# Kernel tuning notes

Measured on AMD Instinct MI355X. Metric: run time of the kernel, lower is better.

The kernel has to match this reference:

```python
import jax, jax.numpy as jnp
import numpy as np

D_MODEL = 1024
NUM_HEADS = 16
HEAD_DIM = D_MODEL // NUM_HEADS  # 64
D_FF = 4096
EPS = 1e-5


def layer_norm(x, gamma, beta):
    mu = jnp.mean(x, axis=-1, keepdims=True)
    var = jnp.mean((x - mu) ** 2, axis=-1, keepdims=True)
    return (x - mu) * jax.lax.rsqrt(var + EPS) * gamma + beta


def apply_rope(t):
    # t: [B, H, S, head_dim]; interleaved-pair rotation as in RoPE.apply_rope
    S, d = t.shape[-2], t.shape[-1]
    inv_freq = 1.0 / (10000.0 ** (jnp.arange(0, d, 2, dtype=jnp.float32) / d))  # [d/2]
    angles = jnp.arange(S, dtype=jnp.float32)[:, None] * inv_freq[None, :]      # [S, d/2]
    sin, cos = jnp.sin(angles), jnp.cos(angles)
    tp = t.reshape(*t.shape[:-1], d // 2, 2)  # pairs of adjacent elements
    t0, t1 = tp[..., 0], tp[..., 1]
    rot = jnp.stack([t0 * cos - t1 * sin, t0 * sin + t1 * cos], axis=-1)
    return rot.reshape(t.shape)


def setup_inputs() -> dict:
    key = jax.random.key(0)
    ks = jax.random.split(key, 18)
    s = 0.02
    d, f = D_MODEL, D_FF
    return {
        "x": jax.random.normal(ks[0], (2, 2048, d), dtype=jnp.float32),
        "Wq": jax.random.normal(ks[1], (d, d), dtype=jnp.float32) * s,
        "bq": jnp.zeros((d,), jnp.float32),
        "Wk": jax.random.normal(ks[2], (d, d), dtype=jnp.float32) * s,
        "bk": jnp.zeros((d,), jnp.float32),
        "Wv": jax.random.normal(ks[3], (d, d), dtype=jnp.float32) * s,
        "bv": jnp.zeros((d,), jnp.float32),
        "Wo": jax.random.normal(ks[4], (d, d), dtype=jnp.float32) * s,
        "bo": jnp.zeros((d,), jnp.float32),
        "W1": jax.random.normal(ks[5], (d, f), dtype=jnp.float32) * s,
        "b1": jnp.zeros((f,), jnp.float32),
        "W2": jax.random.normal(ks[6], (f, d), dtype=jnp.float32) * s,
        "b2": jnp.zeros((d,), jnp.float32),
        "g1": jnp.ones((d,), jnp.float32),
        "beta1": jnp.zeros((d,), jnp.float32),
        "g2": jnp.ones((d,), jnp.float32),
        "beta2": jnp.zeros((d,), jnp.float32),
    }


def reference(x, Wq, bq, Wk, bk, Wv, bv, Wo, bo, W1, b1, W2, b2, g1, beta1, g2, beta2):
    B, S, d = x.shape
    H, hd = NUM_HEADS, HEAD_DIM
    x_norm = layer_norm(x, g1, beta1)
    q = (x_norm @ Wq + bq).reshape(B, S, H, hd).transpose(0, 2, 1, 3)  # [B,H,S,hd]
    k = (x_norm @ Wk + bk).reshape(B, S, H, hd).transpose(0, 2, 1, 3)
    v = (x_norm @ Wv + bv).reshape(B, S, H, hd).transpose(0, 2, 1, 3)
    q = apply_rope(q)
    k = apply_rope(k)
    q = q * (1.0 / jnp.sqrt(jnp.float32(hd)))
    scores = jnp.einsum("bhqd,bhkd->bhqk", q, k)  # [B,H,S,S]
    attn = jax.nn.softmax(scores, axis=-1)
    out = jnp.einsum("bhqk,bhkd->bhqd", attn, v)
    out = out.transpose(0, 2, 1, 3).reshape(B, S, d)
    attn_out = out @ Wo + bo
    x = x + attn_out  # dropout p=0 (eval)
    x_norm2 = layer_norm(x, g2, beta2)
    ffn = jax.nn.relu(x_norm2 @ W1 + b1) @ W2 + b2
    return x + ffn
```

## Files before the change

kernel.cpp:

```cpp
#include <hip/hip_runtime.h>

typedef unsigned short bf16_t;
typedef short short8 __attribute__((ext_vector_type(8)));
typedef float f32x4 __attribute__((ext_vector_type(4)));
typedef float f32x16 __attribute__((ext_vector_type(16)));
typedef unsigned int u32x4 __attribute__((ext_vector_type(4)));

static __device__ __forceinline__ unsigned short f2bf(float f) {
  unsigned int u = __float_as_uint(f);
  unsigned int r = (u + 0x7FFFu + ((u >> 16) & 1u)) >> 16;
  return (unsigned short)r;
}
static __device__ __forceinline__ float bf2f(unsigned short u) {
  return __uint_as_float((unsigned int)u << 16);
}
static __device__ __forceinline__ unsigned int cvt_pk_bf16(float lo, float hi) {
  unsigned int r;
  asm("v_cvt_pk_bf16_f32 %0, %1, %2" : "=v"(r) : "v"(lo), "v"(hi));
  return r;
}
static __device__ __forceinline__ void pl32swap(unsigned int& a, unsigned int& b) {
  asm("v_permlane32_swap_b32 %0, %1" : "+v"(a), "+v"(b));
}

__device__ __forceinline__ void gload_lds16(const void* g, void* l) {
  __builtin_amdgcn_global_load_lds((const __attribute__((address_space(1))) void*)g,
                                   (__attribute__((address_space(3))) void*)l,
                                   16, 0, 0);
}

__global__ __launch_bounds__(256) void prep_kernel(
    const float* __restrict__ Wq, const float* __restrict__ Wk,
    const float* __restrict__ Wv, const float* __restrict__ Wo,
    const float* __restrict__ W1, const float* __restrict__ W2,
    const float* __restrict__ x, const float* __restrict__ g1,
    const float* __restrict__ be1,
    bf16_t* __restrict__ WqkvT, bf16_t* __restrict__ W1T,
    bf16_t* __restrict__ W2T, bf16_t* __restrict__ xnb) {
  __shared__ float tile[32][33];
  const int bid = blockIdx.x;
  if (bid < 12288) {
    const float* src;
    bf16_t* dst;
    int rows, cols, bx, by;
    if (bid < 4096) {
      const int z = bid >> 10, r = bid & 1023;
      src = (z == 0) ? Wq : (z == 1) ? Wk : (z == 2) ? Wv : Wo;
      dst = WqkvT + (size_t)z * 1048576;
      rows = 1024; cols = 1024;
      bx = (r & 31) * 32; by = (r >> 5) * 32;
    } else if (bid < 8192) {
      const int r = bid - 4096;
      src = W1; dst = W1T; rows = 1024; cols = 4096;
      bx = (r & 127) * 32; by = (r >> 7) * 32;
    } else {
      const int r = bid - 8192;
      src = W2; dst = W2T; rows = 4096; cols = 1024;
      bx = (r & 31) * 32; by = (r >> 5) * 32;
    }
    const int tx = threadIdx.x & 31, ty = threadIdx.x >> 5;
#pragma unroll
    for (int i = 0; i < 32; i += 8)
      tile[ty + i][tx] = src[(size_t)(by + ty + i) * cols + (bx + tx)];
    __syncthreads();
#pragma unroll
    for (int i = 0; i < 32; i += 8)
      dst[(size_t)(bx + ty + i) * rows + (by + tx)] = f2bf(tile[tx][ty + i]);
  } else {
    const int row = bid - 12288;
    const int tid = threadIdx.x;
    const float4 v = reinterpret_cast<const float4*>(x + (size_t)row * 1024)[tid];
    float s = v.x + v.y + v.z + v.w;
    float ss = v.x * v.x + v.y * v.y + v.z * v.z + v.w * v.w;
#pragma unroll
    for (int off = 32; off; off >>= 1) {
      s += __shfl_xor(s, off, 64);
      ss += __shfl_xor(ss, off, 64);
    }
    float* red = &tile[0][0];
    const int wave = tid >> 6, lane = tid & 63;
    if (lane == 0) { red[wave] = s; red[4 + wave] = ss; }
    __syncthreads();
    const float mu = (red[0] + red[1] + red[2] + red[3]) * (1.f / 1024.f);
    const float ms = (red[4] + red[5] + red[6] + red[7]) * (1.f / 1024.f);
    const float rstd = rsqrtf(ms - mu * mu + 1e-5f);
    const float4 gg = reinterpret_cast<const float4*>(g1)[tid];
    const float4 bb = reinterpret_cast<const float4*>(be1)[tid];
    bf16_t* o = xnb + (size_t)row * 1024 + tid * 4;
    o[0] = f2bf((v.x - mu) * rstd * gg.x + bb.x);
    o[1] = f2bf((v.y - mu) * rstd * gg.y + bb.y);
    o[2] = f2bf((v.z - mu) * rstd * gg.z + bb.z);
    o[3] = f2bf((v.w - mu) * rstd * gg.w + bb.w);
  }
}

__global__ __launch_bounds__(256) void ln2_combine(const bf16_t* __restrict__ p,
                                                   const float* __restrict__ x,
                                                   const float* __restrict__ bo,
                                                   const float* __restrict__ g,
                                                   const float* __restrict__ be,
                                                   float* __restrict__ x2,
                                                   bf16_t* __restrict__ xn) {
  const int row = blockIdx.x;
  const int tid = threadIdx.x;
  const float4 xv = reinterpret_cast<const float4*>(x + (size_t)row * 1024)[tid];
  const float4 bb = reinterpret_cast<const float4*>(bo)[tid];
  float4 v = {bb.x + xv.x, bb.y + xv.y, bb.z + xv.z, bb.w + xv.w};
#pragma unroll
  for (int z = 0; z < 4; ++z) {
    const ushort4 a = reinterpret_cast<const ushort4*>(p + (size_t)z * 4194304 + (size_t)row * 1024)[tid];
    v.x += bf2f(a.x); v.y += bf2f(a.y); v.z += bf2f(a.z); v.w += bf2f(a.w);
  }
  reinterpret_cast<float4*>(x2 + (size_t)row * 1024)[tid] = v;
  float s = v.x + v.y + v.z + v.w;
  float ss = v.x * v.x + v.y * v.y + v.z * v.z + v.w * v.w;
#pragma unroll
  for (int off = 32; off; off >>= 1) {
    s += __shfl_xor(s, off, 64);
    ss += __shfl_xor(ss, off, 64);
  }
  __shared__ float red[8];
  const int wave = tid >> 6, lane = tid & 63;
  if (lane == 0) { red[wave] = s; red[4 + wave] = ss; }
  __syncthreads();
  const float mu = (red[0] + red[1] + red[2] + red[3]) * (1.f / 1024.f);
  const float ms = (red[4] + red[5] + red[6] + red[7]) * (1.f / 1024.f);
  const float rstd = rsqrtf(ms - mu * mu + 1e-5f);
  const float4 gg = reinterpret_cast<const float4*>(g)[tid];
  const float4 eb = reinterpret_cast<const float4*>(be)[tid];
  bf16_t* o = xn + (size_t)row * 1024 + tid * 4;
  o[0] = f2bf((v.x - mu) * rstd * gg.x + eb.x);
  o[1] = f2bf((v.y - mu) * rstd * gg.y + eb.y);
  o[2] = f2bf((v.z - mu) * rstd * gg.z + eb.z);
  o[3] = f2bf((v.w - mu) * rstd * gg.w + eb.w);
}

__global__ __launch_bounds__(256) void ffn_combine(const bf16_t* __restrict__ p0,
                                                   const bf16_t* __restrict__ p2,
                                                   const float* __restrict__ x2,
                                                   const float* __restrict__ b2,
                                                   float* __restrict__ out) {
  const int row = blockIdx.x;
  const int tid = threadIdx.x;
  const ushort4 a0 = reinterpret_cast<const ushort4*>(p0 + (size_t)row * 1024)[tid];
  const ushort4 a1 = reinterpret_cast<const ushort4*>(p0 + 4194304 + (size_t)row * 1024)[tid];
  const ushort4 a2 = reinterpret_cast<const ushort4*>(p2 + (size_t)row * 1024)[tid];
  const float4 xv = reinterpret_cast<const float4*>(x2 + (size_t)row * 1024)[tid];
  const float4 bb = reinterpret_cast<const float4*>(b2)[tid];
  float4 v;
  v.x = bf2f(a0.x) + bf2f(a1.x) + bf2f(a2.x) + bb.x + xv.x;
  v.y = bf2f(a0.y) + bf2f(a1.y) + bf2f(a2.y) + bb.y + xv.y;
  v.z = bf2f(a0.z) + bf2f(a1.z) + bf2f(a2.z) + bb.z + xv.z;
  v.w = bf2f(a0.w) + bf2f(a1.w) + bf2f(a2.w) + bb.w + xv.w;
  reinterpret_cast<float4*>(out + (size_t)row * 1024)[tid] = v;
}

__global__ __launch_bounds__(256) void rope_bf16(bf16_t* __restrict__ q,
                                                 bf16_t* __restrict__ k) {
  const int id = blockIdx.x * 256 + threadIdx.x;
  const int i = id & 31;
  const int s = (id >> 5) & 2047;
  const int bh = id >> 16;
  const float inv = exp2f((float)i * -0.41524101186f);
  float sn, cs;
  sincosf((float)s * inv, &sn, &cs);
  const size_t base = ((size_t)bh * 2048 + s) * 64 + 2 * i;
  unsigned int qp = *(unsigned int*)&q[base];
  unsigned int kp = *(unsigned int*)&k[base];
  const float q0 = bf2f(qp & 0xffff), q1 = bf2f(qp >> 16);
  const float k0 = bf2f(kp & 0xffff), k1 = bf2f(kp >> 16);
  const float qs = 0.18033688f;
  const unsigned int qo =
      (unsigned int)f2bf((q0 * cs - q1 * sn) * qs) |
      ((unsigned int)f2bf((q0 * sn + q1 * cs) * qs) << 16);
  const unsigned int ko =
      (unsigned int)f2bf(k0 * cs - k1 * sn) |
      ((unsigned int)f2bf(k0 * sn + k1 * cs) << 16);
  *(unsigned int*)&q[base] = qo;
  *(unsigned int*)&k[base] = ko;
}

__global__ __launch_bounds__(256) void vtrans(const bf16_t* __restrict__ v,
                                              bf16_t* __restrict__ vt) {
  __shared__ bf16_t tile[32][33];
  const int bh = blockIdx.x;
  const int s0 = blockIdx.y * 32;
  const int d0 = blockIdx.z * 32;
  const int tx = threadIdx.x & 31, ty = threadIdx.x >> 5;
  const size_t base = (size_t)bh * (2048 * 64);
#pragma unroll
  for (int i = 0; i < 32; i += 8)
    tile[ty + i][tx] = v[base + (size_t)(s0 + ty + i) * 64 + d0 + tx];
  __syncthreads();
#pragma unroll
  for (int i = 0; i < 32; i += 8)
    vt[base + (size_t)(d0 + ty + i) * 2048 + s0 + tx] = tile[tx][ty + i];
}

__global__ __launch_bounds__(256) void attn4(const bf16_t* __restrict__ qb,
                                             const bf16_t* __restrict__ kb,
                                             const bf16_t* __restrict__ vt,
                                             bf16_t* __restrict__ out) {
  const int bh = blockIdx.x;
  const int tid = threadIdx.x, wave = tid >> 6, lane = tid & 63;
  const int l31 = lane & 31, hi = lane >> 5;
  const int q0 = blockIdx.y * 128 + wave * 32;
  const size_t kvb = (size_t)bh * (2048 * 64);

  __shared__ __align__(16) bf16_t Ks[2][4096];
  __shared__ __align__(16) bf16_t Vs[2][4096];
  __shared__ float lred[4][32];

  short8 qf[4];
#pragma unroll
  for (int st = 0; st < 4; ++st)
    qf[st] = *(const short8*)&qb[kvb + (size_t)(q0 + l31) * 64 + st * 16 + hi * 8];

  f32x16 acc0, acc1;
#pragma unroll
  for (int r = 0; r < 16; ++r) { acc0[r] = 0.f; acc1[r] = 0.f; }
  float ls0 = 0.f, ls1 = 0.f, ls2 = 0.f, ls3 = 0.f;

#pragma unroll
  for (int j = 0; j < 2; ++j) {
    const int s = wave * 128 + j * 64 + lane;
    const int r = s >> 3;
    const int c = (s & 7) ^ (r & 7);
    gload_lds16(kb + kvb + (size_t)r * 64 + c * 8, &Ks[0][(size_t)s * 8]);
    gload_lds16(vt + kvb + (size_t)r * 2048 + c * 8, &Vs[0][(size_t)s * 8]);
  }
  __syncthreads();

  for (int t = 0; t < 2048; t += 64) {
    const int cur = (t >> 6) & 1;
    if (t + 64 < 2048) {
#pragma unroll
      for (int j = 0; j < 2; ++j) {
        const int s = wave * 128 + j * 64 + lane;
        const int r = s >> 3;
        const int c = (s & 7) ^ (r & 7);
        gload_lds16(kb + kvb + (size_t)(t + 64 + r) * 64 + c * 8, &Ks[cur ^ 1][(size_t)s * 8]);
        gload_lds16(vt + kvb + (size_t)r * 2048 + (t + 64) + c * 8, &Vs[cur ^ 1][(size_t)s * 8]);
      }
    }
    f32x16 p0, p1;
#pragma unroll
    for (int r = 0; r < 16; ++r) { p0[r] = 0.f; p1[r] = 0.f; }
#pragma unroll
    for (int st = 0; st < 4; ++st) {
      const int R0 = l31, R1 = 32 + l31;
      const short8 kf0 = *(const short8*)&Ks[cur][(size_t)(R0 * 8 + (((st << 1) | hi) ^ (R0 & 7))) * 8];
      const short8 kf1 = *(const short8*)&Ks[cur][(size_t)(R1 * 8 + (((st << 1) | hi) ^ (R1 & 7))) * 8];
      p0 = __builtin_amdgcn_mfma_f32_32x32x16_bf16(kf0, qf[st], p0, 0, 0, 0);
      p1 = __builtin_amdgcn_mfma_f32_32x32x16_bf16(kf1, qf[st], p1, 0, 0, 0);
    }
#pragma unroll
    for (int f = 0; f < 2; ++f) {
      f32x16& p = f ? p1 : p0;
      float e[16];
#pragma unroll
      for (int r = 0; r < 16; ++r) e[r] = exp2f(p[r]);
      ls0 += e[0] + e[1] + e[2] + e[3];
      ls1 += e[4] + e[5] + e[6] + e[7];
      ls2 += e[8] + e[9] + e[10] + e[11];
      ls3 += e[12] + e[13] + e[14] + e[15];
      unsigned int a0 = cvt_pk_bf16(e[0], e[1]), b0 = cvt_pk_bf16(e[4], e[5]);
      unsigned int a1 = cvt_pk_bf16(e[2], e[3]), b1 = cvt_pk_bf16(e[6], e[7]);
      unsigned int a2 = cvt_pk_bf16(e[8], e[9]), b2 = cvt_pk_bf16(e[12], e[13]);
      unsigned int a3 = cvt_pk_bf16(e[10], e[11]), b3 = cvt_pk_bf16(e[14], e[15]);
      pl32swap(a0, b0);
      pl32swap(a1, b1);
      pl32swap(a2, b2);
      pl32swap(a3, b3);
      const u32x4 w0 = {a0, a1, b0, b1};
      const u32x4 w1 = {a2, a3, b2, b3};
      const short8 pf0 = __builtin_bit_cast(short8, w0);
      const short8 pf1 = __builtin_bit_cast(short8, w1);
#pragma unroll
      for (int ks = 0; ks < 2; ++ks) {
        const short8 pf = ks ? pf1 : pf0;
        {
          const int R = l31;
          const int C = (((f << 2) | (ks << 1) | hi) ^ (R & 7));
          const short8 vf = *(const short8*)&Vs[cur][(size_t)(R * 8 + C) * 8];
          acc0 = __builtin_amdgcn_mfma_f32_32x32x16_bf16(pf, vf, acc0, 0, 0, 0);
        }
        {
          const int R = 32 + l31;
          const int C = (((f << 2) | (ks << 1) | hi) ^ (R & 7));
          const short8 vf = *(const short8*)&Vs[cur][(size_t)(R * 8 + C) * 8];
          acc1 = __builtin_amdgcn_mfma_f32_32x32x16_bf16(pf, vf, acc1, 0, 0, 0);
        }
      }
    }
    __syncthreads();
  }

  float lsum = (ls0 + ls1) + (ls2 + ls3);
  lsum += __shfl_xor(lsum, 32, 64);
  if (lane < 32) lred[wave][l31] = lsum;
  __syncthreads();

  const int b = bh >> 4, h = bh & 15;
#pragma unroll
  for (int r = 0; r < 16; ++r) {
    const int qrow = (r & 3) + 8 * (r >> 2) + 4 * hi;
    const float rl = 1.f / lred[wave][qrow];
    const size_t ro = (size_t)(b * 2048 + q0 + qrow) * 1024 + h * 64;
    out[ro + l31] = f2bf(acc0[r] * rl);
    out[ro + 32 + l31] = f2bf(acc1[r] * rl);
  }
}

enum { MODE_QKV = 0, MODE_FF1 = 1, MODE_PART = 2 };

template <int MODE>
__global__ __launch_bounds__(256) void gemm_bt(
    const bf16_t* __restrict__ A, const bf16_t* __restrict__ BT,
    int M, int N, int K, int kspan,
    const float* __restrict__ bias0, const float* __restrict__ bias1,
    const float* __restrict__ bias2,
    bf16_t* __restrict__ ob0, bf16_t* __restrict__ ob1, bf16_t* __restrict__ ob2) {
  __shared__ __align__(16) char smem[34816];
  bf16_t* As = (bf16_t*)smem;
  bf16_t* Bs = (bf16_t*)(smem + 16384);
  const int tid = threadIdx.x;
  const int wave = tid >> 6, lane = tid & 63;
  const int row16 = lane & 15, quad = lane >> 4;
  const int m0 = blockIdx.x * 128, n0 = blockIdx.y * 128;
  const int wm = (wave & 1) << 6, wn = (wave >> 1) << 6;

  f32x4 acc[4][4];
#pragma unroll
  for (int i = 0; i < 4; ++i)
#pragma unroll
    for (int j = 0; j < 4; ++j) acc[i][j] = (f32x4){0.f, 0.f, 0.f, 0.f};

  const int kb = blockIdx.z * kspan;
  const int kend = (kb + kspan < K) ? kb + kspan : K;

  for (int k0 = kb; k0 < kend; k0 += 64) {
#pragma unroll
    for (int j = 0; j < 4; ++j) {
      const int s = j * 256 + tid;
      const int r = s >> 3;
      const int cg = ((s & 7) ^ (r & 7)) << 3;
      gload_lds16(A + (size_t)(m0 + r) * K + k0 + cg, As + (size_t)s * 8);
      gload_lds16(BT + (size_t)(n0 + r) * K + k0 + cg, Bs + (size_t)s * 8);
    }
    __syncthreads();
    const int sw = row16 & 7;
#pragma unroll
    for (int kk = 0; kk < 2; ++kk) {
      short8 af[4], bfr[4];
#pragma unroll
      for (int mi = 0; mi < 4; ++mi)
        af[mi] = *(const short8*)&As[(size_t)(wm + mi * 16 + row16) * 64 + (((kk << 2) | quad) ^ sw) * 8];
#pragma unroll
      for (int ni = 0; ni < 4; ++ni)
        bfr[ni] = *(const short8*)&Bs[(size_t)(wn + ni * 16 + row16) * 64 + (((kk << 2) | quad) ^ sw) * 8];
#pragma unroll
      for (int mi = 0; mi < 4; ++mi)
#pragma unroll
        for (int ni = 0; ni < 4; ++ni)
          acc[mi][ni] =
              __builtin_amdgcn_mfma_f32_16x16x32_bf16(af[mi], bfr[ni], acc[mi][ni], 0, 0, 0);
    }
    __syncthreads();
  }

  bf16_t* ct = (bf16_t*)smem;
#pragma unroll
  for (int mi = 0; mi < 4; ++mi)
#pragma unroll
    for (int ni = 0; ni < 4; ++ni) {
      const int gn = n0 + wn + ni * 16 + row16;
      float bsv = 0.f;
      if (MODE == MODE_QKV)
        bsv = (gn < 1024) ? bias0[gn] : (gn < 2048) ? bias1[gn - 1024] : bias2[gn - 2048];
      else if (MODE == MODE_FF1)
        bsv = bias0[gn];
#pragma unroll
      for (int r = 0; r < 4; ++r) {
        float c = acc[mi][ni][r] + bsv;
        if (MODE == MODE_FF1) c = fmaxf(c, 0.f);
        ct[(size_t)(wm + mi * 16 + quad * 4 + r) * 136 + wn + ni * 16 + row16] = f2bf(c);
      }
    }
  __syncthreads();
  const int lr0 = tid >> 4, lc = tid & 15;
#pragma unroll
  for (int i = 0; i < 8; ++i) {
    const int lr = i * 16 + lr0;
    const uint4 v = *(const uint4*)&ct[(size_t)lr * 136 + lc * 8];
    const int gm = m0 + lr;
    if (MODE == MODE_QKV) {
      const int nn = (n0 & 1023) + lc * 8;
      const int h = nn >> 6, d = nn & 63;
      const int b = gm >> 11, s = gm & 2047;
      bf16_t* dst = (n0 < 1024) ? ob0 : (n0 < 2048) ? ob1 : ob2;
      *(uint4*)&dst[(((size_t)b * 16 + h) * 2048 + s) * 64 + d] = v;
    } else if (MODE == MODE_FF1) {
      *(uint4*)&ob0[(size_t)gm * N + n0 + lc * 8] = v;
    } else {
      bf16_t* dst = (blockIdx.z == 2) ? ob1 : ob0 + (size_t)blockIdx.z * 4194304;
      *(uint4*)&dst[(size_t)gm * N + n0 + lc * 8] = v;
    }
  }
}

extern "C" void kernel_launch(void* const* d_in, const int* in_sizes, int n_in,
                              void* d_out, int out_size, void* d_ws, size_t ws_size,
                              hipStream_t stream) {
  const float* x = (const float*)d_in[0];
  const float* Wq = (const float*)d_in[1];
  const float* bq = (const float*)d_in[2];
  const float* Wk = (const float*)d_in[3];
  const float* bk = (const float*)d_in[4];
  const float* Wv = (const float*)d_in[5];
  const float* bv = (const float*)d_in[6];
  const float* Wo = (const float*)d_in[7];
  const float* bo = (const float*)d_in[8];
  const float* W1 = (const float*)d_in[9];
  const float* b1 = (const float*)d_in[10];
  const float* W2 = (const float*)d_in[11];
  const float* b2 = (const float*)d_in[12];
  const float* g1 = (const float*)d_in[13];
  const float* be1 = (const float*)d_in[14];
  const float* g2 = (const float*)d_in[15];
  const float* be2 = (const float*)d_in[16];
  float* out = (float*)d_out;

  char* ws = (char*)d_ws;
  size_t off = 0;
  auto alloc = [&](size_t bytes) {
    void* p = ws + off;
    off += (bytes + 255) & ~(size_t)255;
    return p;
  };
  bf16_t* WqkvT = (bf16_t*)alloc(3072ULL * 1024 * 2);
  bf16_t* WoT = (bf16_t*)alloc(1024ULL * 1024 * 2);
  bf16_t* W1T = (bf16_t*)alloc(4096ULL * 1024 * 2);
  bf16_t* W2T = (bf16_t*)alloc(1024ULL * 4096 * 2);
  bf16_t* xnb = (bf16_t*)alloc(4096ULL * 1024 * 2);
  bf16_t* qb = (bf16_t*)alloc(4194304ULL * 2);
  bf16_t* kb = (bf16_t*)alloc(4194304ULL * 2);
  bf16_t* vraw = (bf16_t*)alloc(4194304ULL * 2);
  bf16_t* vt = (bf16_t*)alloc(4194304ULL * 2);
  bf16_t* h1 = qb;
  bf16_t* x2p = qb;
  bf16_t* ffp = WqkvT;
  float* x2 = (float*)alloc(16777216ULL);

  prep_kernel<<<16384, 256, 0, stream>>>(Wq, Wk, Wv, Wo, W1, W2, x, g1, be1,
                                         WqkvT, W1T, W2T, xnb);

  gemm_bt<MODE_QKV><<<dim3(32, 24, 1), 256, 0, stream>>>(xnb, WqkvT, 4096, 3072, 1024, 1024,
                                                         bq, bk, bv, qb, kb, vraw);

  rope_bf16<<<8192, 256, 0, stream>>>(qb, kb);

  vtrans<<<dim3(32, 64, 2), 256, 0, stream>>>(vraw, vt);

  attn4<<<dim3(32, 16), 256, 0, stream>>>(qb, kb, vt, xnb);

  gemm_bt<MODE_PART><<<dim3(32, 8, 4), 256, 0, stream>>>(xnb, WoT, 4096, 1024, 1024, 256,
                                                         nullptr, nullptr, nullptr,
                                                         x2p, x2p + 2 * 4194304, nullptr);

  ln2_combine<<<4096, 256, 0, stream>>>(x2p, x, bo, g2, be2, x2, xnb);

  gemm_bt<MODE_FF1><<<dim3(32, 32, 1), 256, 0, stream>>>(xnb, W1T, 4096, 4096, 1024, 1024,
                                                         b1, nullptr, nullptr,
                                                         h1, nullptr, nullptr);

  gemm_bt<MODE_PART><<<dim3(32, 8, 3), 256, 0, stream>>>(h1, W2T, 4096, 1024, 4096, 1408,
                                                         nullptr, nullptr, nullptr,
                                                         ffp, xnb, nullptr);

  ffn_combine<<<4096, 256, 0, stream>>>(ffp, xnb, x2, b2, out);
}
```

Before: 374.1 us.

## Compute softmax row sums via MFMA with ones, unroll attention loop by two

```diff
diff --git a/kernel.cpp b/kernel.cpp
--- a/kernel.cpp
+++ b/kernel.cpp
@@ -197,10 +197,10 @@
     vt[base + (size_t)(d0 + ty + i) * 2048 + s0 + tx] = tile[tx][ty + i];
 }
 
-__global__ __launch_bounds__(256) void attn4(const bf16_t* __restrict__ qb,
-                                             const bf16_t* __restrict__ kb,
-                                             const bf16_t* __restrict__ vt,
-                                             bf16_t* __restrict__ out) {
+__global__ __launch_bounds__(256, 2) void attn5(const bf16_t* __restrict__ qb,
+                                                const bf16_t* __restrict__ kb,
+                                                const bf16_t* __restrict__ vt,
+                                                bf16_t* __restrict__ out) {
   const int bh = blockIdx.x;
   const int tid = threadIdx.x, wave = tid >> 6, lane = tid & 63;
   const int l31 = lane & 31, hi = lane >> 5;
@@ -209,17 +209,35 @@
 
   __shared__ __align__(16) bf16_t Ks[2][4096];
   __shared__ __align__(16) bf16_t Vs[2][4096];
-  __shared__ float lred[4][32];
 
   short8 qf[4];
 #pragma unroll
   for (int st = 0; st < 4; ++st)
     qf[st] = *(const short8*)&qb[kvb + (size_t)(q0 + l31) * 64 + st * 16 + hi * 8];
 
-  f32x16 acc0, acc1;
-#pragma unroll
-  for (int r = 0; r < 16; ++r) { acc0[r] = 0.f; acc1[r] = 0.f; }
-  float ls0 = 0.f, ls1 = 0.f, ls2 = 0.f, ls3 = 0.f;
+  int kidx[2][4];
+  int vidx[2][2][2];
+#pragma unroll
+  for (int st = 0; st < 4; ++st) {
+    const int R0 = l31, R1 = 32 + l31;
+    kidx[0][st] = (R0 * 8 + (((st << 1) | hi) ^ (R0 & 7))) * 8;
+    kidx[1][st] = (R1 * 8 + (((st << 1) | hi) ^ (R1 & 7))) * 8;
+  }
+#pragma unroll
+  for (int f = 0; f < 2; ++f)
+#pragma unroll
+    for (int ks = 0; ks < 2; ++ks) {
+      const int R0 = l31, R1 = 32 + l31;
+      vidx[0][f][ks] = (R0 * 8 + (((f << 2) | (ks << 1) | hi) ^ (R0 & 7))) * 8;
+      vidx[1][f][ks] = (R1 * 8 + (((f << 2) | (ks << 1) | hi) ^ (R1 & 7))) * 8;
+    }
+
+  short8 vones;
+#pragma unroll
+  for (int j = 0; j < 8; ++j) vones[j] = (short)0x3F80;
+
+  f32x16 acc0 = {}, acc1 = {}, lacc = {};
+  const f32x16 fz = {};
 
 #pragma unroll
   for (int j = 0; j < 2; ++j) {
@@ -231,81 +249,77 @@
   }
   __syncthreads();
 
-  for (int t = 0; t < 2048; t += 64) {
-    const int cur = (t >> 6) & 1;
-    if (t + 64 < 2048) {
-#pragma unroll
-      for (int j = 0; j < 2; ++j) {
-        const int s = wave * 128 + j * 64 + lane;
-        const int r = s >> 3;
-        const int c = (s & 7) ^ (r & 7);
-        gload_lds16(kb + kvb + (size_t)(t + 64 + r) * 64 + c * 8, &Ks[cur ^ 1][(size_t)s * 8]);
-        gload_lds16(vt + kvb + (size_t)r * 2048 + (t + 64) + c * 8, &Vs[cur ^ 1][(size_t)s * 8]);
-      }
-    }
-    f32x16 p0, p1;
-#pragma unroll
-    for (int r = 0; r < 16; ++r) { p0[r] = 0.f; p1[r] = 0.f; }
-#pragma unroll
-    for (int st = 0; st < 4; ++st) {
-      const int R0 = l31, R1 = 32 + l31;
-      const short8 kf0 = *(const short8*)&Ks[cur][(size_t)(R0 * 8 + (((st << 1) | hi) ^ (R0 & 7))) * 8];
-      const short8 kf1 = *(const short8*)&Ks[cur][(size_t)(R1 * 8 + (((st << 1) | hi) ^ (R1 & 7))) * 8];
-      p0 = __builtin_amdgcn_mfma_f32_32x32x16_bf16(kf0, qf[st], p0, 0, 0, 0);
-      p1 = __builtin_amdgcn_mfma_f32_32x32x16_bf16(kf1, qf[st], p1, 0, 0, 0);
-    }
-#pragma unroll
-    for (int f = 0; f < 2; ++f) {
-      f32x16& p = f ? p1 : p0;
-      float e[16];
-#pragma unroll
-      for (int r = 0; r < 16; ++r) e[r] = exp2f(p[r]);
-      ls0 += e[0] + e[1] + e[2] + e[3];
-      ls1 += e[4] + e[5] + e[6] + e[7];
-      ls2 += e[8] + e[9] + e[10] + e[11];
-      ls3 += e[12] + e[13] + e[14] + e[15];
-      unsigned int a0 = cvt_pk_bf16(e[0], e[1]), b0 = cvt_pk_bf16(e[4], e[5]);
-      unsigned int a1 = cvt_pk_bf16(e[2], e[3]), b1 = cvt_pk_bf16(e[6], e[7]);
-      unsigned int a2 = cvt_pk_bf16(e[8], e[9]), b2 = cvt_pk_bf16(e[12], e[13]);
-      unsigned int a3 = cvt_pk_bf16(e[10], e[11]), b3 = cvt_pk_bf16(e[14], e[15]);
-      pl32swap(a0, b0);
-      pl32swap(a1, b1);
-      pl32swap(a2, b2);
-      pl32swap(a3, b3);
-      const u32x4 w0 = {a0, a1, b0, b1};
-      const u32x4 w1 = {a2, a3, b2, b3};
-      const short8 pf0 = __builtin_bit_cast(short8, w0);
-      const short8 pf1 = __builtin_bit_cast(short8, w1);
-#pragma unroll
-      for (int ks = 0; ks < 2; ++ks) {
-        const short8 pf = ks ? pf1 : pf0;
-        {
-          const int R = l31;
-          const int C = (((f << 2) | (ks << 1) | hi) ^ (R & 7));
-          const short8 vf = *(const short8*)&Vs[cur][(size_t)(R * 8 + C) * 8];
-          acc0 = __builtin_amdgcn_mfma_f32_32x32x16_bf16(pf, vf, acc0, 0, 0, 0);
-        }
-        {
-          const int R = 32 + l31;
-          const int C = (((f << 2) | (ks << 1) | hi) ^ (R & 7));
-          const short8 vf = *(const short8*)&Vs[cur][(size_t)(R * 8 + C) * 8];
-          acc1 = __builtin_amdgcn_mfma_f32_32x32x16_bf16(pf, vf, acc1, 0, 0, 0);
-        }
-      }
-    }
-    __syncthreads();
-  }
-
-  float lsum = (ls0 + ls1) + (ls2 + ls3);
-  lsum += __shfl_xor(lsum, 32, 64);
-  if (lane < 32) lred[wave][l31] = lsum;
-  __syncthreads();
+#define ATTN_TILE(BUF, TPREF, DOPREF)                                                     \
+  {                                                                                       \
+    if (DOPREF) {                                                                         \
+      _Pragma("unroll") for (int j = 0; j < 2; ++j) {                                     \
+        const int s = wave * 128 + j * 64 + lane;                                         \
+        const int r = s >> 3;                                                             \
+        const int c = (s & 7) ^ (r & 7);                                                  \
+        gload_lds16(kb + kvb + (size_t)((TPREF) + r) * 64 + c * 8,                        \
+                    &Ks[(BUF) ^ 1][(size_t)s * 8]);                                       \
+        gload_lds16(vt + kvb + (size_t)r * 2048 + (TPREF) + c * 8,                        \
+                    &Vs[(BUF) ^ 1][(size_t)s * 8]);                                       \
+      }                                                                                   \
+    }                                                                                     \
+    short8 kfa[4], kfb[4];                                                                \
+    _Pragma("unroll") for (int st = 0; st < 4; ++st) {                                    \
+      kfa[st] = *(const short8*)&Ks[BUF][kidx[0][st]];                                    \
+      kfb[st] = *(const short8*)&Ks[BUF][kidx[1][st]];                                    \
+    }                                                                                     \
+    __builtin_amdgcn_s_setprio(1);                                                        \
+    f32x16 p0 = __builtin_amdgcn_mfma_f32_32x32x16_bf16(kfa[0], qf[0], fz, 0, 0, 0);      \
+    f32x16 p1 = __builtin_amdgcn_mfma_f32_32x32x16_bf16(kfb[0], qf[0], fz, 0, 0, 0);      \
+    _Pragma("unroll") for (int st = 1; st < 4; ++st) {                                    \
+      p0 = __builtin_amdgcn_mfma_f32_32x32x16_bf16(kfa[st], qf[st], p0, 0, 0, 0);         \
+      p1 = __builtin_amdgcn_mfma_f32_32x32x16_bf16(kfb[st], qf[st], p1, 0, 0, 0);         \
+    }                                                                                     \
+    __builtin_amdgcn_s_setprio(0);                                                        \
+    _Pragma("unroll") for (int f = 0; f < 2; ++f) {                                       \
+      f32x16& p = f ? p1 : p0;                                                            \
+      float e[16];                                                                        \
+      _Pragma("unroll") for (int r = 0; r < 16; ++r) e[r] = exp2f(p[r]);                  \
+      unsigned int a0 = cvt_pk_bf16(e[0], e[1]), b0 = cvt_pk_bf16(e[4], e[5]);            \
+      unsigned int a1 = cvt_pk_bf16(e[2], e[3]), b1 = cvt_pk_bf16(e[6], e[7]);            \
+      unsigned int a2 = cvt_pk_bf16(e[8], e[9]), b2 = cvt_pk_bf16(e[12], e[13]);          \
+      unsigned int a3 = cvt_pk_bf16(e[10], e[11]), b3 = cvt_pk_bf16(e[14], e[15]);        \
+      pl32swap(a0, b0);                                                                   \
+      pl32swap(a1, b1);                                                                   \
+      pl32swap(a2, b2);                                                                   \
+      pl32swap(a3, b3);                                                                   \
+      const u32x4 w0 = {a0, a1, b0, b1};                                                  \
+      const u32x4 w1 = {a2, a3, b2, b3};                                                  \
+      const short8 pf0 = __builtin_bit_cast(short8, w0);                                  \
+      const short8 pf1 = __builtin_bit_cast(short8, w1);                                  \
+      const short8 vf00 = *(const short8*)&Vs[BUF][vidx[0][f][0]];                        \
+      const short8 vf10 = *(const short8*)&Vs[BUF][vidx[1][f][0]];                        \
+      const short8 vf01 = *(const short8*)&Vs[BUF][vidx[0][f][1]];                        \
+      const short8 vf11 = *(const short8*)&Vs[BUF][vidx[1][f][1]];                        \
+      __builtin_amdgcn_s_setprio(1);                                                      \
+      lacc = __builtin_amdgcn_mfma_f32_32x32x16_bf16(pf0, vones, lacc, 0, 0, 0);          \
+      acc0 = __builtin_amdgcn_mfma_f32_32x32x16_bf16(pf0, vf00, acc0, 0, 0, 0);           \
+      acc1 = __builtin_amdgcn_mfma_f32_32x32x16_bf16(pf0, vf10, acc1, 0, 0, 0);           \
+      lacc = __builtin_amdgcn_mfma_f32_32x32x16_bf16(pf1, vones, lacc, 0, 0, 0);          \
+      acc0 = __builtin_amdgcn_mfma_f32_32x32x16_bf16(pf1, vf01, acc0, 0, 0, 0);           \
+      acc1 = __builtin_amdgcn_mfma_f32_32x32x16_bf16(pf1, vf11, acc1, 0, 0, 0);           \
+      __builtin_amdgcn_s_setprio(0);                                                      \
+    }                                                                                     \
+    __syncthreads();                                                                      \
+  }
+
+  for (int t = 0; t < 1920; t += 128) {
+    ATTN_TILE(0, t + 64, 1)
+    ATTN_TILE(1, t + 128, 1)
+  }
+  ATTN_TILE(0, 1984, 1)
+  ATTN_TILE(1, 0, 0)
+#undef ATTN_TILE
 
   const int b = bh >> 4, h = bh & 15;
 #pragma unroll
   for (int r = 0; r < 16; ++r) {
     const int qrow = (r & 3) + 8 * (r >> 2) + 4 * hi;
-    const float rl = 1.f / lred[wave][qrow];
+    const float rl = 1.f / lacc[r];
     const size_t ro = (size_t)(b * 2048 + q0 + qrow) * 1024 + h * 64;
     out[ro + l31] = f2bf(acc0[r] * rl);
     out[ro + 32 + l31] = f2bf(acc1[r] * rl);
@@ -462,7 +476,7 @@
 
   vtrans<<<dim3(32, 64, 2), 256, 0, stream>>>(vraw, vt);
 
-  attn4<<<dim3(32, 16), 256, 0, stream>>>(qb, kb, vt, xnb);
+  attn5<<<dim3(32, 16), 256, 0, stream>>>(qb, kb, vt, xnb);
 
   gemm_bt<MODE_PART><<<dim3(32, 8, 4), 256, 0, stream>>>(xnb, WoT, 4096, 1024, 1024, 256,
                                                          nullptr, nullptr, nullptr,
```

Result: faster. 365.3 us (-2.4%).
